# Kernel tuning notes

Measured on AMD Instinct MI355X. Metric: run time of the kernel, lower is better.

## Reference

```python
import jax, jax.numpy as jnp
import numpy as np

N, C, T, V = 32, 128, 128, 25
HS, HT, CI = 3, 2, 32
BN_INV = float(1.0 / np.sqrt(1.0 + 1e-5))  # eval-mode BN: running_mean=0, running_var=1


def conv1x1(x, w, b):
    # x: (N,C,T,V), w: (O,C), b: (O,)
    return jnp.einsum('nctv,oc->notv', x, w) + b[None, :, None, None]


def bn(x, g, b):
    return x * (g * BN_INV)[None, :, None, None] + b[None, :, None, None]


def lrelu(x):
    return jax.nn.leaky_relu(x, 0.1)


def setup_inputs() -> dict:
    key = jax.random.key(0)
    ks = jax.random.split(key, 16)
    w = lambda k, shp: jax.random.normal(k, shp, dtype=jnp.float32) * 0.05
    inp = {
        'x': jax.random.normal(ks[0], (N, C, T, V), dtype=jnp.float32),
        # spatial attention QK projection (conv 1x1): 2*HS*CI out channels
        'w_in_s': w(ks[1], (2 * HS * CI, C)), 'b_in_s': jnp.zeros((2 * HS * CI,), jnp.float32),
        'attention0s': jnp.ones((1, HS, V, V), jnp.float32) / V,
        'alphas': jnp.ones((1, HS, 1, 1), jnp.float32),
        'w_out_s': w(ks[2], (C, HS * C)), 'b_out_s': jnp.zeros((C,), jnp.float32),
        'g_out_s': jnp.ones((C,), jnp.float32), 'be_out_s': jnp.zeros((C,), jnp.float32),
        'w_ff_s': w(ks[3], (C, C)), 'b_ff_s': jnp.zeros((C,), jnp.float32),
        'g_ff_s': jnp.ones((C,), jnp.float32), 'be_ff_s': jnp.zeros((C,), jnp.float32),
        # temporal attention QK projection: 4*HT*CI out channels
        'w_in_t': w(ks[4], (4 * HT * CI, C)), 'b_in_t': jnp.zeros((4 * HT * CI,), jnp.float32),
        'alphat_f': jnp.ones((1, HT, 1, 1), jnp.float32),
        'alphat_b': jnp.ones((1, HT, 1, 1), jnp.float32),
        'w_out_t': w(ks[5], (C, 2 * HT * C)), 'b_out_t': jnp.zeros((C,), jnp.float32),
        'g_out_t': jnp.ones((C,), jnp.float32), 'be_out_t': jnp.zeros((C,), jnp.float32),
        'w_ff_t': w(ks[6], (C, C)), 'b_ff_t': jnp.zeros((C,), jnp.float32),
        'g_ff_t': jnp.ones((C,), jnp.float32), 'be_ff_t': jnp.zeros((C,), jnp.float32),
        # TCN: 7x1 temporal conv
        'w_tcn': w(ks[7], (C, C, 7, 1)), 'b_tcn': jnp.zeros((C,), jnp.float32),
        'g_tcn': jnp.ones((C,), jnp.float32), 'be_tcn': jnp.zeros((C,), jnp.float32),
    }
    return inp


def reference(x, w_in_s, b_in_s, attention0s, alphas, w_out_s, b_out_s, g_out_s, be_out_s,
              w_ff_s, b_ff_s, g_ff_s, be_ff_s, w_in_t, b_in_t, alphat_f, alphat_b,
              w_out_t, b_out_t, g_out_t, be_out_t, w_ff_t, b_ff_t, g_ff_t, be_ff_t,
              w_tcn, b_tcn, g_tcn, be_tcn):
    n = x.shape[0]
    # ---------------- spatial attention (S_atten='free', glo_reg_s) ----------------
    att_bias = attention0s[:, :, None]            # (1,HS,1,V,V) broadcast over T
    alphas_u = alphas[:, :, None]                 # (1,HS,1,1,1)
    qk = conv1x1(x, w_in_s, b_in_s).reshape(n, 2 * HS, CI, T, V)
    q, k = qk[:, :HS], qk[:, HS:]
    att = att_bias + jnp.tanh(jnp.einsum('nsctu,nsctv->nstuv', q, k) / CI) * alphas_u  # (N,HS,T,V,V)
    y = jnp.einsum('nctu,nstuv->nsctv', x, att).reshape(n, HS * C, T, V)
    y = bn(conv1x1(y, w_out_s, b_out_s), g_out_s, be_out_s)
    y = lrelu(x + y)                               # downs1 = identity (in==out, stride 1)
    y = bn(conv1x1(y, w_ff_s, b_ff_s), g_ff_s, be_ff_s)
    s_out = lrelu(x + y)                           # downs2 = identity
    # ---------------- temporal attention (directed, T_atten='context') ----------------
    z_in = s_out                                   # parallel=False -> temporal eats s_out
    qk_t = conv1x1(z_in, w_in_t, b_in_t).reshape(n, 4 * HT, CI, T, V)
    qt, kt = qk_t[:, :2 * HT], qk_t[:, 2 * HT:]
    qt = qt.mean(-1)                               # context attention: mean over joints -> (N,2HT,CI,T)
    kt = kt.mean(-1)
    att_t = jnp.tanh(jnp.einsum('nsct,nscu->nstu', qt, kt) / CI)  # (N,2HT,T,T)
    backward_mask = jnp.triu(jnp.ones((T, T), jnp.float32))
    forward_mask = backward_mask.T
    att_f = att_t[:, :HT] * alphat_f * forward_mask
    att_b = att_t[:, HT:] * alphat_b * backward_mask
    att_t = jnp.concatenate([att_f, att_b], axis=1)               # (N,2HT,T,T)
    z = jnp.einsum('nctv,nstu->nscuv', z_in, att_t).reshape(n, 2 * HT * C, T, V)
    z = bn(conv1x1(z, w_out_t, b_out_t), g_out_t, be_out_t)
    z = lrelu(z_in + z)                            # downt1 = identity
    z = bn(conv1x1(z, w_ff_t, b_ff_t), g_ff_t, be_ff_t)
    t_out = lrelu(z_in + z)                        # downt2 = identity
    # ---------------- TCN branch ----------------
    z2 = jax.lax.conv_general_dilated(t_out, w_tcn, (1, 1), ((3, 3), (0, 0)),
                                      dimension_numbers=('NCHW', 'OIHW', 'NCHW'))
    z2 = bn(z2 + b_tcn[None, :, None, None] * 0 + b_tcn[None, :, None, None], g_tcn, be_tcn) if False else bn(z2 + b_tcn[None, :, None, None], g_tcn, be_tcn)
    out = lrelu(t_out + z2)                        # downtTCN = identity
    return out
```

## Files before the change

### kernel.cpp

```cpp
#include <hip/hip_runtime.h>
#include <cstddef>

#define Nn 32
#define Cc 128
#define Tt 128
#define Vv 25
#define BN_INV 0.9999950000374997f


typedef __attribute__((ext_vector_type(8))) short bf16x8;
typedef __attribute__((ext_vector_type(4))) short short4v;
typedef __attribute__((ext_vector_type(4))) float f32x4;

__device__ __forceinline__ unsigned short f2bf(float f) {
    union { float f; unsigned u; } x; x.f = f;
    return (unsigned short)((x.u + 0x7FFFu + ((x.u >> 16) & 1u)) >> 16);
}
__device__ __forceinline__ float bf2f(unsigned short s) {
    union { unsigned u; float f; } x; x.u = ((unsigned)s) << 16;
    return x.f;
}


#define GFETCH(K0)                                                             \
    {                                                                          \
        int mg = m0 + sm;                                                      \
        if (mg < M) {                                                          \
            const unsigned short* ap = An + (size_t)mg*lda + (K0) + skh*16;    \
            a0n = *(const bf16x8*)ap;                                          \
            a1n = *(const bf16x8*)(ap + 8);                                    \
        }                                                                      \
        if (BMODE == 0) {                                                      \
            const unsigned short* Bn = (const unsigned short*)Bv               \
                                     + (size_t)n*bn_stride;                    \
            _Pragma("unroll")                                                  \
            for (int j = 0; j < 8; ++j)                                        \
                bqn[j] = Bn[(size_t)((K0) + skq*8 + j)*ldb + bcol];            \
        } else if (BMODE == 4) {                                               \
            const float* Bf = (const float*)Bv + (size_t)n*bn_stride;          \
            _Pragma("unroll")                                                  \
            for (int j = 0; j < 8; ++j)                                        \
                bqn[j] = f2bf(Bf[(size_t)((K0) + skq*8 + j)*ldb + bcol]);      \
        } else if (BMODE == 1) {                                               \
            const unsigned short* Bn = (const unsigned short*)Bv               \
                                     + (size_t)n*bn_stride;                    \
            int kb = (K0) + skq*8;                                             \
            int kidx = kb >> 7, c0 = kb & 127;                                 \
            int e = bcol + (kidx - 3)*25;                                      \
            bool ok = ((unsigned)e < 3200u);                                   \
            _Pragma("unroll")                                                  \
            for (int j = 0; j < 8; ++j)                                        \
                bqn[j] = ok ? Bn[(size_t)(c0 + j)*3200 + e] : (unsigned short)0;\
        } else if (BMODE == 3) {                                               \
            const unsigned short* Bn = (const unsigned short*)Bv               \
                                     + (size_t)n*bn_stride;                    \
            int kb = (K0) + skq*8;                                             \
            int h = kb >> 7, t0b = kb & 127;                                   \
            const unsigned short* bp = Bn + (size_t)h*409600 + (size_t)bo*3200 \
                                          + (size_t)t0b*25 + bv_;              \
            _Pragma("unroll")                                                  \
            for (int j = 0; j < 8; ++j) bqn[j] = bp[j*25];                     \
        } else if (BMODE == 6) {                                               \
            const unsigned short* Bn = (const unsigned short*)Bv               \
                                     + (size_t)n*bn_stride;                    \
            *(bf16x8*)bqn = *(const bf16x8*)(Bn + (size_t)bcol*ldb             \
                                             + (K0) + skq*8);                  \
        } else {                                                  \
            const unsigned short* Bn = (const unsigned short*)Bv               \
                                     + (size_t)n*bn_stride;                    \
            int kb = (K0) + skq*8;                                             \
            int kidx = kb >> 7, c0 = kb & 127;                                 \
            long e = (long)bcol + (long)(kidx - 3)*25;                         \
            *(bf16x8*)bqn = *(const bf16x8*)(Bn + e*128 + c0);                 \
        }                                                                      \
    }

template<int BMODE, int DMODE, int OM>
__global__ __launch_bounds__(256, 4) void gemm_k(
    const unsigned short* __restrict__ A, const void* __restrict__ Bv,
    float* __restrict__ D, unsigned short* __restrict__ Dbf,
    const float* __restrict__ resp, const float* __restrict__ bias,
    const float* __restrict__ gg, const float* __restrict__ bb,
    int M, int K, int lda, int ldb, int ldd,
    long an_stride, long bn_stride, long dn_stride, long dbfn,
    int gn, int gxn)
{
    __shared__ short Al[8*64*8];
    __shared__ short Bl[4*64*8];
    __shared__ __attribute__((aligned(16))) short Ot[(DMODE==1) ? 64*136 : 4];

    const int nwg = gridDim.x;
    const int b   = blockIdx.x;
    const int w   = (b & 7)*(nwg >> 3) + (b >> 3);
    const int n   = w / gxn;
    const int rem = w - n*gxn;
    const int mt  = rem / gn;
    const int nt  = rem - mt*gn;
    const int m0 = mt*128;
    const int j0 = nt*64;

    const unsigned short* An = A + (size_t)n*an_stride;

    const int tid = threadIdx.x;
    const int wav = tid >> 6, lane = tid & 63;
    const int lq = lane >> 4, l16 = lane & 15;

    const int sm  = tid >> 1, skh = tid & 1;
    const int scol = tid & 63, skq = tid >> 6;
    const int bcol = j0 + scol;

    int bo = 0, bv_ = 0;
    if (BMODE == 3) { bo = bcol/25; bv_ = bcol - 25*bo; }

    f32x4 acc[2][4];
    #pragma unroll
    for (int i = 0; i < 2; ++i)
        #pragma unroll
        for (int c = 0; c < 4; ++c) acc[i][c] = (f32x4){0.f,0.f,0.f,0.f};

    bf16x8 a0n = (bf16x8){0,0,0,0,0,0,0,0}, a1n = a0n;
    alignas(16) unsigned short bqn[8];
    GFETCH(0);

    for (int k0 = 0; k0 < K; k0 += 32) {
        __syncthreads();
        {
            short* Ap = Al + ((size_t)((sm>>4)*64 + (sm&15) + 32*skh))*8;
            *(bf16x8*)Ap = a0n;
            *(bf16x8*)(Ap + 128) = a1n;
        }
        {
            short* Bp = Bl + ((size_t)((scol>>4)*64 + skq*16 + (scol&15)))*8;
            *(bf16x8*)Bp = *(const bf16x8*)bqn;
        }
        __syncthreads();

        if (k0 + 32 < K) GFETCH(k0 + 32);

        bf16x8 afr[2], bfr[4];
        afr[0] = *(const bf16x8*)(Al + ((size_t)((2*wav+0)*64 + lane))*8);
        afr[1] = *(const bf16x8*)(Al + ((size_t)((2*wav+1)*64 + lane))*8);
        #pragma unroll
        for (int c = 0; c < 4; ++c)
            bfr[c] = *(const bf16x8*)(Bl + ((size_t)(c*64 + lane))*8);
        #pragma unroll
        for (int i = 0; i < 2; ++i)
            #pragma unroll
            for (int c = 0; c < 4; ++c)
                acc[i][c] = __builtin_amdgcn_mfma_f32_16x16x32_bf16(
                    afr[i], bfr[c], acc[i][c], 0, 0, 0);
    }

    if (DMODE == 1) {
        #pragma unroll
        for (int i = 0; i < 2; ++i) {
            const int mbase = (2*wav + i)*16 + lq*4;
            #pragma unroll
            for (int ct = 0; ct < 4; ++ct) {
                const int col = j0 + ct*16 + l16;
                short4v pk;
                #pragma unroll
                for (int r = 0; r < 4; ++r) {
                    const int mg = mbase + r;
                    const size_t addr = (size_t)mg*ldd + col + (size_t)n*dn_stride;
                    float val = acc[i][ct][r] + (bias ? bias[mg] : 0.f);
                    if (gg) {
                        val = val*(gg[mg]*BN_INV) + bb[mg] + resp[addr];
                        val = val > 0.f ? val : 0.1f*val;
                    }
                    if (OM != 1) D[addr] = val;
                    pk[r] = (short)f2bf(val);
                }
                *(short4v*)(Ot + (ct*16 + l16)*136 + mbase) = pk;
            }
        }
        __syncthreads();
        #pragma unroll
        for (int j = 0; j < 4; ++j) {
            int idx = j*256 + tid;
            int cl = idx >> 4, m8 = (idx & 15)*8;
            *(bf16x8*)(Dbf + (size_t)(j0 + cl)*128 + m8 + (size_t)n*dbfn)
                = *(const bf16x8*)(Ot + cl*136 + m8);
        }
    } else {
        #pragma unroll
        for (int i = 0; i < 2; ++i) {
            const int mbase = m0 + (2*wav + i)*16 + lq*4;
            #pragma unroll
            for (int ct = 0; ct < 4; ++ct) {
                const int col = j0 + ct*16 + l16;
                if (DMODE == 0) {
                    #pragma unroll
                    for (int r = 0; r < 4; ++r) {
                        const int mg = mbase + r;
                        if (mg < M) {
                            const size_t addr = (size_t)mg*ldd + col
                                              + (size_t)n*dn_stride;
                            float val = acc[i][ct][r] + (bias ? bias[mg] : 0.f);
                            if (gg) {
                                val = val*(gg[mg]*BN_INV) + bb[mg] + resp[addr];
                                val = val > 0.f ? val : 0.1f*val;
                            }
                            if (OM != 1) D[addr] = val;
                            if (OM >= 1) Dbf[addr] = f2bf(val);
                        }
                    }
                } else {
                    const int c = col/25, v = col - 25*c;
                    const float bi = bias ? bias[c] : 0.f;
                    float gv = 0.f, b2 = 0.f;
                    if (gg) { gv = gg[c]*BN_INV; b2 = bb[c]; }
                    #pragma unroll
                    for (int r = 0; r < 4; ++r) {
                        const int u = mbase + r;
                        const size_t addr = (size_t)c*3200 + (size_t)u*25 + v
                                          + (size_t)n*dn_stride;
                        float val = acc[i][ct][r] + bi;
                        if (gg) {
                            val = val*gv + b2 + resp[addr];
                            val = val > 0.f ? val : 0.1f*val;
                        }
                        if (OM != 1) D[addr] = val;
                        if (OM >= 1) Dbf[addr] = f2bf(val);
                    }
                }
            }
        }
    }
}

__global__ void k_prep(const float* __restrict__ wis, const float* __restrict__ wos,
                       const float* __restrict__ wfs, const float* __restrict__ wit,
                       const float* __restrict__ wot, const float* __restrict__ wft,
                       const float* __restrict__ wtc, unsigned short* __restrict__ W) {
    int i = blockIdx.x*256 + threadIdx.x;
    if (i < 24576) { W[i] = f2bf(wis[i]); return; }          i -= 24576;
    if (i < 49152) { W[24576 + i] = f2bf(wos[i]); return; }  i -= 49152;
    if (i < 16384) { W[73728 + i] = f2bf(wfs[i]); return; }  i -= 16384;
    if (i < 32768) { W[90112 + i] = f2bf(wit[i]); return; }  i -= 32768;
    if (i < 65536) {
        int ho = i >> 7, c = i & 127; int h = ho >> 7, o = ho & 127;
        W[122880 + i] = f2bf(wot[o*512 + h*128 + c]); return; } i -= 65536;
    if (i < 16384) { W[188416 + i] = f2bf(wft[i]); return; } i -= 16384;
    if (i < 114688) {
        int o = i / 896; int r = i - o*896; int kidx = r >> 7, c = r & 127;
        W[204800 + i] = f2bf(wtc[(o*128 + c)*7 + kidx]); }
}

__global__ void k_zpad(unsigned short* __restrict__ p) {
    int i = blockIdx.x*256 + threadIdx.x;
    if (i >= 76800) return;
    int chunk = i*8;
    int n = chunk / 19200;
    int r = chunk - n*19200;
    size_t addr = (size_t)n*428800 + (size_t)(r < 9600 ? r : 419200 + (r - 9600));
    *(bf16x8*)(p + addr) = (bf16x8){0,0,0,0,0,0,0,0};
}

__global__ void k_att_s(const unsigned short* __restrict__ qk,
                        const float* __restrict__ att0,
                        const float* __restrict__ alphas,
                        unsigned short* __restrict__ att) {
    int b = blockIdx.x;
    int n = b / (3*Tt); int rem = b - n*(3*Tt); int s = rem / Tt; int t = rem - s*Tt;
    __shared__ float qs[32*Vv], ks[32*Vv];
    const unsigned short* qp = qk + (size_t)n*614400 + (size_t)(s*32)*3200 + t*25;
    const unsigned short* kp = qk + (size_t)n*614400 + (size_t)(96 + s*32)*3200 + t*25;
    for (int i = threadIdx.x; i < 32*Vv; i += 256) {
        int c = i / Vv, v = i - c*Vv;
        qs[i] = bf2f(qp[(size_t)c*3200 + v]);
        ks[i] = bf2f(kp[(size_t)c*3200 + v]);
    }
    __syncthreads();
    float alpha = alphas[s];
    for (int i = threadIdx.x; i < Vv*Vv; i += 256) {
        int u = i / Vv, v = i - u*Vv;
        float a = 0.f;
        #pragma unroll
        for (int c = 0; c < 32; ++c) a += qs[c*Vv + u] * ks[c*Vv + v];
        att[(size_t)n*240000 + (size_t)s*80000 + (size_t)t*625 + i] =
            f2bf(att0[s*625 + i] + tanhf(a * (1.f/32.f)) * alpha);
    }
}

__global__ __launch_bounds__(256, 2) void k_eins_mfma(
    const float* __restrict__ X, const unsigned short* __restrict__ att,
    unsigned short* __restrict__ y2)
{
    __shared__ short Xf[128*128];
    __shared__ short Bf[7*4*64*8];

    const int n  = blockIdx.x >> 5;
    const int t0 = (blockIdx.x & 31) * 4;
    const int tid = threadIdx.x;
    const int wav = tid >> 6, lane = tid & 63;
    const int lq = lane >> 4, l16 = lane & 15;

    for (int i = tid; i < 7*4*64; i += 256)
        *(bf16x8*)(Bf + (size_t)i*8) = (bf16x8){0,0,0,0,0,0,0,0};

    const float* xp = X + (size_t)n*409600;
    for (int i = tid; i < 8192; i += 256) {
        int u2 = (i & 15)*2, tl = (i >> 4) & 3, c = i >> 6;
        float f0 = 0.f, f1 = 0.f;
        if (u2 < 25) {
            const float* p = xp + (size_t)c*3200 + (t0 + tl)*25 + u2;
            f0 = p[0];
            if (u2 < 24) f1 = p[1];
        }
        unsigned pk = (unsigned)f2bf(f0) | ((unsigned)f2bf(f1) << 16);
        int byte = (i*4) ^ ((c & 7) << 4);
        *(unsigned*)((char*)Xf + byte) = pk;
    }
    __syncthreads();

    bf16x8 afr[2][4];
    #pragma unroll
    for (int i = 0; i < 2; ++i) {
        const int c = (2*wav + i)*16 + l16;
        #pragma unroll
        for (int ks = 0; ks < 4; ++ks) {
            int byte = ((c*128 + ks*32 + lq*8)*2) ^ ((c & 7) << 4);
            afr[i][ks] = *(const bf16x8*)((const char*)Xf + byte);
        }
    }

    for (int s = 0; s < 3; ++s) {
        const unsigned short* ap = att + (size_t)n*240000 + (size_t)s*80000
                                       + (size_t)t0*625;
        for (int j = tid; j < 2500; j += 256) {
            int tl = j / 625, r = j - tl*625;
            int u = r / 25, v = r - u*25;
            int col = tl*25 + v;
            int l = ((u >> 3) << 4) | (col & 15);
            int nt = col >> 4;
            Bf[(size_t)((nt*4 + tl)*64 + l)*8 + (u & 7)] = (short)ap[j];
        }
        __syncthreads();

        f32x4 acc[2][7];
        #pragma unroll
        for (int i = 0; i < 2; ++i)
            #pragma unroll
            for (int nt = 0; nt < 7; ++nt) acc[i][nt] = (f32x4){0.f,0.f,0.f,0.f};

        #pragma unroll
        for (int ks = 0; ks < 4; ++ks) {
            bf16x8 bfr[7];
            #pragma unroll
            for (int nt = 0; nt < 7; ++nt)
                bfr[nt] = *(const bf16x8*)(Bf + (size_t)((nt*4 + ks)*64 + lane)*8);
            #pragma unroll
            for (int i = 0; i < 2; ++i)
                #pragma unroll
                for (int nt = 0; nt < 7; ++nt)
                    acc[i][nt] = __builtin_amdgcn_mfma_f32_16x16x32_bf16(
                        afr[i][ks], bfr[nt], acc[i][nt], 0, 0, 0);
        }

        unsigned short* yb = y2 + (size_t)n*1228800;
        #pragma unroll
        for (int i = 0; i < 2; ++i) {
            const int row = (2*wav + i)*16 + lq*4;
            #pragma unroll
            for (int nt = 0; nt < 7; ++nt) {
                const int col = nt*16 + l16;
                if (col < 100) {
                    short4v pk;
                    #pragma unroll
                    for (int r = 0; r < 4; ++r) pk[r] = (short)f2bf(acc[i][nt][r]);
                    *(short4v*)(yb + (size_t)(t0*25 + col)*384 + s*128 + row) = pk;
                }
            }
        }
        __syncthreads();
    }
}

__global__ void k_mean(const float* __restrict__ X, unsigned short* __restrict__ xb) {
    int idx = blockIdx.x*256 + threadIdx.x;
    if (idx >= Nn*Cc*Tt) return;
    const float* p = X + (size_t)idx*25;
    float s = 0.f;
    #pragma unroll
    for (int v = 0; v < Vv; ++v) s += p[v];
    int n = idx >> 14, rem = idx & 16383, c = rem >> 7, t = rem & 127;
    xb[(size_t)n*16384 + (size_t)t*128 + c] = f2bf(s * (1.f/25.f));
}

__global__ void k_att_t(const float* __restrict__ qkt, const float* __restrict__ af,
                        const float* __restrict__ ab, unsigned short* __restrict__ attb) {
    int n = blockIdx.x >> 2, h = blockIdx.x & 3;
    __shared__ float qs[32*Tt], ks[32*Tt];
    const float* qp = qkt + (size_t)n*32768 + (size_t)(h*32)*128;
    const float* kp = qkt + (size_t)n*32768 + (size_t)(128 + h*32)*128;
    for (int i = threadIdx.x; i < 32*Tt; i += 256) { qs[i] = qp[i]; ks[i] = kp[i]; }
    __syncthreads();
    float alpha = (h < 2) ? af[h] : ab[h-2];
    for (int i = threadIdx.x; i < Tt*Tt; i += 256) {
        int u = i >> 7, t = i & 127;
        bool keep = (h < 2) ? (t >= u) : (t <= u);
        float val = 0.f;
        if (keep) {
            float a = 0.f;
            #pragma unroll
            for (int c = 0; c < 32; ++c) a += qs[c*Tt + t] * ks[c*Tt + u];
            val = tanhf(a * (1.f/32.f)) * alpha;
        }
        attb[(size_t)n*65536 + (size_t)u*512 + h*128 + t] = f2bf(val);
    }
}

extern "C" void kernel_launch(void* const* d_in, const int* in_sizes, int n_in,
                              void* d_out, int out_size, void* d_ws, size_t ws_size,
                              hipStream_t stream) {
    const float* x       = (const float*)d_in[0];
    const float* w_in_s  = (const float*)d_in[1];
    const float* b_in_s  = (const float*)d_in[2];
    const float* att0s   = (const float*)d_in[3];
    const float* alphas  = (const float*)d_in[4];
    const float* w_out_s = (const float*)d_in[5];
    const float* b_out_s = (const float*)d_in[6];
    const float* g_out_s = (const float*)d_in[7];
    const float* be_out_s= (const float*)d_in[8];
    const float* w_ff_s  = (const float*)d_in[9];
    const float* b_ff_s  = (const float*)d_in[10];
    const float* g_ff_s  = (const float*)d_in[11];
    const float* be_ff_s = (const float*)d_in[12];
    const float* w_in_t  = (const float*)d_in[13];
    const float* b_in_t  = (const float*)d_in[14];
    const float* alphat_f= (const float*)d_in[15];
    const float* alphat_b= (const float*)d_in[16];
    const float* w_out_t = (const float*)d_in[17];
    const float* b_out_t = (const float*)d_in[18];
    const float* g_out_t = (const float*)d_in[19];
    const float* be_out_t= (const float*)d_in[20];
    const float* w_ff_t  = (const float*)d_in[21];
    const float* b_ff_t  = (const float*)d_in[22];
    const float* g_ff_t  = (const float*)d_in[23];
    const float* be_ff_t = (const float*)d_in[24];
    const float* w_tcn   = (const float*)d_in[25];
    const float* b_tcn   = (const float*)d_in[26];
    const float* g_tcn   = (const float*)d_in[27];
    const float* be_tcn  = (const float*)d_in[28];

    float* ws = (float*)d_ws;
    unsigned short* WB    = (unsigned short*)ws;
    unsigned short* QKBF  = (unsigned short*)(ws + 200000);
    unsigned short* S1BF  = (unsigned short*)(ws + 200000);
    unsigned short* ATSB  = (unsigned short*)(ws + 10030400);
    unsigned short* Y2BF  = (unsigned short*)(ws + 13870400);
    unsigned short* TOUTBP= (unsigned short*)(ws + 23710000);
    unsigned short* TOUTB = TOUTBP + 9600;
    float*          SOUT  = ws + 33531200;
    unsigned short* ATTB  = (unsigned short*)(ws + 200000);
    unsigned short* XBARB = (unsigned short*)(ws + 1300000);
    float*          QKT   = ws + 1600000;
    unsigned short* TMPB  = (unsigned short*)(ws + 2700000);
    unsigned short* T1BF  = (unsigned short*)(ws + 46638400);
    float*          TOUT  = ws + 2700000;
    float* out = (float*)d_out;

    unsigned short* wbis = WB;
    unsigned short* wbos = WB + 24576;
    unsigned short* wbfs = WB + 73728;
    unsigned short* wbit = WB + 90112;
    unsigned short* wbot = WB + 122880;
    unsigned short* wbft = WB + 188416;
    unsigned short* wbtc = WB + 204800;

    dim3 blk(256);
    const float* NUL = nullptr;

    k_prep<<<1248, blk, 0, stream>>>(w_in_s, w_out_s, w_ff_s, w_in_t,
                                     w_out_t, w_ff_t, w_tcn, WB);

    gemm_k<4,0,1><<<3200, blk, 0, stream>>>(
        wbis, x, nullptr, QKBF, NUL, b_in_s, NUL, NUL,
        192, 128, 128, 3200, 3200, 0L, 409600L, 614400L, 614400L, 50, 100);
    k_att_s<<<Nn*3*Tt, blk, 0, stream>>>(QKBF, att0s, alphas, ATSB);
    k_eins_mfma<<<dim3(Nn*32), blk, 0, stream>>>(x, ATSB, Y2BF);
    gemm_k<6,1,1><<<1600, blk, 0, stream>>>(
        wbos, Y2BF, nullptr, S1BF, x, b_out_s, g_out_s, be_out_s,
        128, 384, 384, 384, 3200, 0L, 1228800L, 409600L, 409600L, 50, 50);
    gemm_k<6,0,0><<<1600, blk, 0, stream>>>(
        wbfs, S1BF, SOUT, nullptr, x, b_ff_s, g_ff_s, be_ff_s,
        128, 128, 128, 128, 3200, 0L, 409600L, 409600L, 409600L, 50, 50);

    k_mean<<<2048, blk, 0, stream>>>(SOUT, XBARB);
    gemm_k<6,0,0><<<128, blk, 0, stream>>>(
        wbit, XBARB, QKT, nullptr, NUL, b_in_t, NUL, NUL,
        256, 128, 128, 128, 128, 0L, 16384L, 32768L, 32768L, 2, 4);
    k_att_t<<<Nn*4, blk, 0, stream>>>(QKT, alphat_f, alphat_b, ATTB);
    gemm_k<4,0,1><<<6400, blk, 0, stream>>>(
        wbot, SOUT, nullptr, TMPB, NUL, NUL, NUL, NUL,
        512, 128, 128, 3200, 3200, 0L, 409600L, 1638400L, 1638400L, 50, 200);
    gemm_k<3,2,1><<<1600, blk, 0, stream>>>(
        ATTB, TMPB, nullptr, T1BF, SOUT, b_out_t, g_out_t, be_out_t,
        128, 512, 512, 3200, 3200, 65536L, 1638400L, 409600L, 409600L, 50, 50);
    k_zpad<<<300, blk, 0, stream>>>(TOUTBP);
    gemm_k<0,1,2><<<1600, blk, 0, stream>>>(
        wbft, T1BF, TOUT, TOUTB, SOUT, b_ff_t, g_ff_t, be_ff_t,
        128, 128, 128, 3200, 3200, 0L, 409600L, 409600L, 428800L, 50, 50);

    gemm_k<7,0,0><<<1600, blk, 0, stream>>>(
        wbtc, TOUTB, out, nullptr, TOUT, b_tcn, g_tcn, be_tcn,
        128, 896, 896, 0, 3200, 0L, 428800L, 409600L, 409600L, 50, 50);
}
```

Baseline: 706.3 us.

## Add LDS-free register-direct MFMA GEMM for K-contiguous B operand modes

Adds a new GEMM kernel, gemm_nb, that loads A and B fragments straight from global memory into registers in MFMA operand layout. It skips LDS staging and block barriers in the main loop and double-buffers the loads across K steps. The K-contiguous launches (BMODE 6 and the TCN BMODE 7) now use it, and the now-unused B-mode branches are removed from the old kernel's fetch macro. This trades LDS traffic and syncs for redundant global/L2 loads across waves and less latency hiding.

```diff
diff --git a/kernel.cpp b/kernel.cpp
--- a/kernel.cpp
+++ b/kernel.cpp
@@ -21,6 +21,138 @@
     return x.f;
 }
 
+template<int BMODE, int DMODE, int OM>
+__global__ __launch_bounds__(256, 4) void gemm_nb(
+    const unsigned short* __restrict__ A, const void* __restrict__ Bv,
+    float* __restrict__ D, unsigned short* __restrict__ Dbf,
+    const float* __restrict__ resp, const float* __restrict__ bias,
+    const float* __restrict__ gg, const float* __restrict__ bb,
+    int M, int K, int lda, int ldb, int ldd,
+    long an_stride, long bn_stride, long dn_stride, long dbfn,
+    int gn, int gxn)
+{
+    __shared__ __attribute__((aligned(16))) short Ot[(DMODE==1) ? 64*136 : 4];
+
+    const int nwg = gridDim.x;
+    const int b   = blockIdx.x;
+    const int w   = (b & 7)*(nwg >> 3) + (b >> 3);
+    const int n   = w / gxn;
+    const int rem = w - n*gxn;
+    const int mt  = rem / gn;
+    const int nt  = rem - mt*gn;
+    const int m0 = mt*128;
+    const int j0 = nt*64;
+
+    const int tid = threadIdx.x;
+    const int wav = tid >> 6, lane = tid & 63;
+    const int lq = lane >> 4, l16 = lane & 15;
+
+    const unsigned short* An = A + (size_t)n*an_stride;
+    const unsigned short* Bn = (const unsigned short*)Bv + (size_t)n*bn_stride;
+
+    const unsigned short* pa0 = An + (size_t)(m0 + (2*wav+0)*16 + l16)*lda + lq*8;
+    const unsigned short* pa1 = An + (size_t)(m0 + (2*wav+1)*16 + l16)*lda + lq*8;
+    const unsigned short* pb[4];
+    #pragma unroll
+    for (int c = 0; c < 4; ++c) {
+        const int col = j0 + c*16 + l16;
+        pb[c] = (BMODE == 6) ? Bn + (size_t)col*ldb + lq*8
+                             : Bn + ((long)col - 75)*128 + lq*8;
+    }
+
+    f32x4 acc[2][4];
+    #pragma unroll
+    for (int i = 0; i < 2; ++i)
+        #pragma unroll
+        for (int c = 0; c < 4; ++c) acc[i][c] = (f32x4){0.f,0.f,0.f,0.f};
+
+#define OFFB(K0) ((BMODE == 6) ? (long)(K0) \
+                               : ((long)((K0) >> 7)*3200 + (long)((K0) & 127)))
+#define LOADF(K0, A0, A1, BF)                                                  \
+    {                                                                          \
+        A0 = *(const bf16x8*)(pa0 + (K0));                                     \
+        A1 = *(const bf16x8*)(pa1 + (K0));                                     \
+        const long ob = OFFB(K0);                                              \
+        _Pragma("unroll")                                                      \
+        for (int c = 0; c < 4; ++c) BF[c] = *(const bf16x8*)(pb[c] + ob);      \
+    }
+#define MFMA8(A0, A1, BF)                                                      \
+    {                                                                          \
+        _Pragma("unroll")                                                      \
+        for (int c = 0; c < 4; ++c) {                                          \
+            acc[0][c] = __builtin_amdgcn_mfma_f32_16x16x32_bf16(               \
+                A0, BF[c], acc[0][c], 0, 0, 0);                                \
+            acc[1][c] = __builtin_amdgcn_mfma_f32_16x16x32_bf16(               \
+                A1, BF[c], acc[1][c], 0, 0, 0);                                \
+        }                                                                      \
+    }
+
+    bf16x8 aA0, aA1, bA[4], aB0, aB1, bB[4];
+    LOADF(0, aA0, aA1, bA);
+    for (int k0 = 0; k0 < K; k0 += 64) {
+        if (k0 + 32 < K) LOADF(k0 + 32, aB0, aB1, bB);
+        MFMA8(aA0, aA1, bA);
+        if (k0 + 64 < K) LOADF(k0 + 64, aA0, aA1, bA);
+        if (k0 + 32 < K) MFMA8(aB0, aB1, bB);
+    }
+#undef OFFB
+#undef LOADF
+#undef MFMA8
+
+    if (DMODE == 1) {
+        #pragma unroll
+        for (int i = 0; i < 2; ++i) {
+            const int mbase = (2*wav + i)*16 + lq*4;
+            #pragma unroll
+            for (int ct = 0; ct < 4; ++ct) {
+                const int col = j0 + ct*16 + l16;
+                short4v pk;
+                #pragma unroll
+                for (int r = 0; r < 4; ++r) {
+                    const int mg = mbase + r;
+                    const size_t addr = (size_t)mg*ldd + col + (size_t)n*dn_stride;
+                    float val = acc[i][ct][r] + (bias ? bias[mg] : 0.f);
+                    if (gg) {
+                        val = val*(gg[mg]*BN_INV) + bb[mg] + resp[addr];
+                        val = val > 0.f ? val : 0.1f*val;
+                    }
+                    if (OM != 1) D[addr] = val;
+                    pk[r] = (short)f2bf(val);
+                }
+                *(short4v*)(Ot + (ct*16 + l16)*136 + mbase) = pk;
+            }
+        }
+        __syncthreads();
+        #pragma unroll
+        for (int j = 0; j < 4; ++j) {
+            int idx = j*256 + tid;
+            int cl = idx >> 4, m8 = (idx & 15)*8;
+            *(bf16x8*)(Dbf + (size_t)(j0 + cl)*128 + m8 + (size_t)n*dbfn)
+                = *(const bf16x8*)(Ot + cl*136 + m8);
+        }
+    } else {
+        #pragma unroll
+        for (int i = 0; i < 2; ++i) {
+            const int mbase = m0 + (2*wav + i)*16 + lq*4;
+            #pragma unroll
+            for (int ct = 0; ct < 4; ++ct) {
+                const int col = j0 + ct*16 + l16;
+                #pragma unroll
+                for (int r = 0; r < 4; ++r) {
+                    const int mg = mbase + r;
+                    const size_t addr = (size_t)mg*ldd + col + (size_t)n*dn_stride;
+                    float val = acc[i][ct][r] + (bias ? bias[mg] : 0.f);
+                    if (gg) {
+                        val = val*(gg[mg]*BN_INV) + bb[mg] + resp[addr];
+                        val = val > 0.f ? val : 0.1f*val;
+                    }
+                    if (OM != 1) D[addr] = val;
+                    if (OM >= 1) Dbf[addr] = f2bf(val);
+                }
+            }
+        }
+    }
+}
 
 #define GFETCH(K0)                                                             \
     {                                                                          \
@@ -41,17 +173,7 @@
             _Pragma("unroll")                                                  \
             for (int j = 0; j < 8; ++j)                                        \
                 bqn[j] = f2bf(Bf[(size_t)((K0) + skq*8 + j)*ldb + bcol]);      \
-        } else if (BMODE == 1) {                                               \
-            const unsigned short* Bn = (const unsigned short*)Bv               \
-                                     + (size_t)n*bn_stride;                    \
-            int kb = (K0) + skq*8;                                             \
-            int kidx = kb >> 7, c0 = kb & 127;                                 \
-            int e = bcol + (kidx - 3)*25;                                      \
-            bool ok = ((unsigned)e < 3200u);                                   \
-            _Pragma("unroll")                                                  \
-            for (int j = 0; j < 8; ++j)                                        \
-                bqn[j] = ok ? Bn[(size_t)(c0 + j)*3200 + e] : (unsigned short)0;\
-        } else if (BMODE == 3) {                                               \
+        } else {                                                  \
             const unsigned short* Bn = (const unsigned short*)Bv               \
                                      + (size_t)n*bn_stride;                    \
             int kb = (K0) + skq*8;                                             \
@@ -60,18 +182,6 @@
                                           + (size_t)t0b*25 + bv_;              \
             _Pragma("unroll")                                                  \
             for (int j = 0; j < 8; ++j) bqn[j] = bp[j*25];                     \
-        } else if (BMODE == 6) {                                               \
-            const unsigned short* Bn = (const unsigned short*)Bv               \
-                                     + (size_t)n*bn_stride;                    \
-            *(bf16x8*)bqn = *(const bf16x8*)(Bn + (size_t)bcol*ldb             \
-                                             + (K0) + skq*8);                  \
-        } else {                                                  \
-            const unsigned short* Bn = (const unsigned short*)Bv               \
-                                     + (size_t)n*bn_stride;                    \
-            int kb = (K0) + skq*8;                                             \
-            int kidx = kb >> 7, c0 = kb & 127;                                 \
-            long e = (long)bcol + (long)(kidx - 3)*25;                         \
-            *(bf16x8*)bqn = *(const bf16x8*)(Bn + e*128 + c0);                 \
         }                                                                      \
     }
 
@@ -480,15 +590,15 @@
         192, 128, 128, 3200, 3200, 0L, 409600L, 614400L, 614400L, 50, 100);
     k_att_s<<<Nn*3*Tt, blk, 0, stream>>>(QKBF, att0s, alphas, ATSB);
     k_eins_mfma<<<dim3(Nn*32), blk, 0, stream>>>(x, ATSB, Y2BF);
-    gemm_k<6,1,1><<<1600, blk, 0, stream>>>(
+    gemm_nb<6,1,1><<<1600, blk, 0, stream>>>(
         wbos, Y2BF, nullptr, S1BF, x, b_out_s, g_out_s, be_out_s,
         128, 384, 384, 384, 3200, 0L, 1228800L, 409600L, 409600L, 50, 50);
-    gemm_k<6,0,0><<<1600, blk, 0, stream>>>(
+    gemm_nb<6,0,0><<<1600, blk, 0, stream>>>(
         wbfs, S1BF, SOUT, nullptr, x, b_ff_s, g_ff_s, be_ff_s,
         128, 128, 128, 128, 3200, 0L, 409600L, 409600L, 409600L, 50, 50);
 
     k_mean<<<2048, blk, 0, stream>>>(SOUT, XBARB);
-    gemm_k<6,0,0><<<128, blk, 0, stream>>>(
+    gemm_nb<6,0,0><<<128, blk, 0, stream>>>(
         wbit, XBARB, QKT, nullptr, NUL, b_in_t, NUL, NUL,
         256, 128, 128, 128, 128, 0L, 16384L, 32768L, 32768L, 2, 4);
     k_att_t<<<Nn*4, blk, 0, stream>>>(QKT, alphat_f, alphat_b, ATTB);
@@ -503,7 +613,7 @@
         wbft, T1BF, TOUT, TOUTB, SOUT, b_ff_t, g_ff_t, be_ff_t,
         128, 128, 128, 3200, 3200, 0L, 409600L, 409600L, 428800L, 50, 50);
 
-    gemm_k<7,0,0><<<1600, blk, 0, stream>>>(
+    gemm_nb<7,0,0><<<1600, blk, 0, stream>>>(
         wbtc, TOUTB, out, nullptr, TOUT, b_tcn, g_tcn, be_tcn,
         128, 896, 896, 0, 3200, 0L, 428800L, 409600L, 409600L, 50, 50);
 }
```

New measurement: 800.7 us. 13.4% more time.

## Fuse spatial out-projection and feedforward GEMMs into one kernel via LDS

Applied to the files above, without the earlier changes.

Replaces the two back-to-back spatial-branch GEMMs (out projection with BN/residual/leaky-relu, then feedforward 1x1 conv) with a single kernel. The intermediate bf16 tile stays in LDS and feeds the second MFMA GEMM directly instead of going through global memory. This removes one launch and the write and read of the S1 intermediate. In exchange the kernel uses more LDS and registers per block, and the unused BMODE 1 path is deleted.

```diff
diff --git a/kernel.cpp b/kernel.cpp
--- a/kernel.cpp
+++ b/kernel.cpp
@@ -20,7 +20,6 @@
     union { unsigned u; float f; } x; x.u = ((unsigned)s) << 16;
     return x.f;
 }
-
 
 #define GFETCH(K0)                                                             \
     {                                                                          \
@@ -41,16 +40,6 @@
             _Pragma("unroll")                                                  \
             for (int j = 0; j < 8; ++j)                                        \
                 bqn[j] = f2bf(Bf[(size_t)((K0) + skq*8 + j)*ldb + bcol]);      \
-        } else if (BMODE == 1) {                                               \
-            const unsigned short* Bn = (const unsigned short*)Bv               \
-                                     + (size_t)n*bn_stride;                    \
-            int kb = (K0) + skq*8;                                             \
-            int kidx = kb >> 7, c0 = kb & 127;                                 \
-            int e = bcol + (kidx - 3)*25;                                      \
-            bool ok = ((unsigned)e < 3200u);                                   \
-            _Pragma("unroll")                                                  \
-            for (int j = 0; j < 8; ++j)                                        \
-                bqn[j] = ok ? Bn[(size_t)(c0 + j)*3200 + e] : (unsigned short)0;\
         } else if (BMODE == 3) {                                               \
             const unsigned short* Bn = (const unsigned short*)Bv               \
                                      + (size_t)n*bn_stride;                    \
@@ -229,6 +218,150 @@
     }
 }
 
+__global__ __launch_bounds__(256, 4) void k_s1ff(
+    const unsigned short* __restrict__ A1, const unsigned short* __restrict__ B1,
+    const unsigned short* __restrict__ A2,
+    float* __restrict__ D, const float* __restrict__ xresp,
+    const float* __restrict__ b1, const float* __restrict__ g1,
+    const float* __restrict__ bb1,
+    const float* __restrict__ b2, const float* __restrict__ g2,
+    const float* __restrict__ bb2)
+{
+    __shared__ short Al[8*64*8];
+    __shared__ short Bl[4*64*8];
+    __shared__ __attribute__((aligned(16))) short Ilds[64*136];
+
+    const int nwg = gridDim.x;
+    const int b   = blockIdx.x;
+    const int w   = (b & 7)*(nwg >> 3) + (b >> 3);
+    const int n   = w / 50;
+    const int nt  = w - n*50;
+    const int j0  = nt*64;
+
+    const int tid = threadIdx.x;
+    const int wav = tid >> 6, lane = tid & 63;
+    const int lq = lane >> 4, l16 = lane & 15;
+
+    const int sm  = tid >> 1, skh = tid & 1;
+    const int scol = tid & 63, skq = tid >> 6;
+    const int bcol = j0 + scol;
+
+    const unsigned short* Bn = B1 + (size_t)n*1228800;
+
+    f32x4 acc[2][4];
+    #pragma unroll
+    for (int i = 0; i < 2; ++i)
+        #pragma unroll
+        for (int c = 0; c < 4; ++c) acc[i][c] = (f32x4){0.f,0.f,0.f,0.f};
+
+    bf16x8 a0n, a1n;
+    alignas(16) unsigned short bqn[8];
+    {
+        const unsigned short* ap = A1 + (size_t)sm*384 + skh*16;
+        a0n = *(const bf16x8*)ap;
+        a1n = *(const bf16x8*)(ap + 8);
+        *(bf16x8*)bqn = *(const bf16x8*)(Bn + (size_t)bcol*384 + skq*8);
+    }
+
+    for (int k0 = 0; k0 < 384; k0 += 32) {
+        __syncthreads();
+        {
+            short* Ap = Al + ((size_t)((sm>>4)*64 + (sm&15) + 32*skh))*8;
+            *(bf16x8*)Ap = a0n;
+            *(bf16x8*)(Ap + 128) = a1n;
+        }
+        {
+            short* Bp = Bl + ((size_t)((scol>>4)*64 + skq*16 + (scol&15)))*8;
+            *(bf16x8*)Bp = *(const bf16x8*)bqn;
+        }
+        __syncthreads();
+
+        if (k0 + 32 < 384) {
+            const unsigned short* ap = A1 + (size_t)sm*384 + (k0+32) + skh*16;
+            a0n = *(const bf16x8*)ap;
+            a1n = *(const bf16x8*)(ap + 8);
+            *(bf16x8*)bqn = *(const bf16x8*)(Bn + (size_t)bcol*384 + (k0+32) + skq*8);
+        }
+
+        bf16x8 afr[2], bfr[4];
+        afr[0] = *(const bf16x8*)(Al + ((size_t)((2*wav+0)*64 + lane))*8);
+        afr[1] = *(const bf16x8*)(Al + ((size_t)((2*wav+1)*64 + lane))*8);
+        #pragma unroll
+        for (int c = 0; c < 4; ++c)
+            bfr[c] = *(const bf16x8*)(Bl + ((size_t)(c*64 + lane))*8);
+        #pragma unroll
+        for (int i = 0; i < 2; ++i)
+            #pragma unroll
+            for (int c = 0; c < 4; ++c)
+                acc[i][c] = __builtin_amdgcn_mfma_f32_16x16x32_bf16(
+                    afr[i], bfr[c], acc[i][c], 0, 0, 0);
+    }
+
+    __syncthreads();
+    #pragma unroll
+    for (int i = 0; i < 2; ++i) {
+        const int mbase = (2*wav + i)*16 + lq*4;
+        #pragma unroll
+        for (int ct = 0; ct < 4; ++ct) {
+            const int col = j0 + ct*16 + l16;
+            short4v pk;
+            #pragma unroll
+            for (int r = 0; r < 4; ++r) {
+                const int mg = mbase + r;
+                const size_t addr = (size_t)mg*3200 + col + (size_t)n*409600;
+                float val = acc[i][ct][r] + b1[mg];
+                val = val*(g1[mg]*BN_INV) + bb1[mg] + xresp[addr];
+                val = val > 0.f ? val : 0.1f*val;
+                pk[r] = (short)f2bf(val);
+            }
+            *(short4v*)(Ilds + (ct*16 + l16)*136 + mbase) = pk;
+        }
+    }
+    __syncthreads();
+
+    f32x4 acc2[2][4];
+    #pragma unroll
+    for (int i = 0; i < 2; ++i)
+        #pragma unroll
+        for (int c = 0; c < 4; ++c) acc2[i][c] = (f32x4){0.f,0.f,0.f,0.f};
+
+    #pragma unroll
+    for (int k2 = 0; k2 < 128; k2 += 32) {
+        bf16x8 a2[2], b2f[4];
+        #pragma unroll
+        for (int i = 0; i < 2; ++i)
+            a2[i] = *(const bf16x8*)(A2 + (size_t)((2*wav+i)*16 + l16)*128
+                                        + k2 + lq*8);
+        #pragma unroll
+        for (int c = 0; c < 4; ++c)
+            b2f[c] = *(const bf16x8*)(Ilds + (c*16 + l16)*136 + k2 + lq*8);
+        #pragma unroll
+        for (int i = 0; i < 2; ++i)
+            #pragma unroll
+            for (int c = 0; c < 4; ++c)
+                acc2[i][c] = __builtin_amdgcn_mfma_f32_16x16x32_bf16(
+                    a2[i], b2f[c], acc2[i][c], 0, 0, 0);
+    }
+
+    #pragma unroll
+    for (int i = 0; i < 2; ++i) {
+        const int mbase = (2*wav + i)*16 + lq*4;
+        #pragma unroll
+        for (int ct = 0; ct < 4; ++ct) {
+            const int col = j0 + ct*16 + l16;
+            #pragma unroll
+            for (int r = 0; r < 4; ++r) {
+                const int mg = mbase + r;
+                const size_t addr = (size_t)mg*3200 + col + (size_t)n*409600;
+                float val = acc2[i][ct][r] + b2[mg];
+                val = val*(g2[mg]*BN_INV) + bb2[mg] + xresp[addr];
+                val = val > 0.f ? val : 0.1f*val;
+                D[addr] = val;
+            }
+        }
+    }
+}
+
 __global__ void k_prep(const float* __restrict__ wis, const float* __restrict__ wos,
                        const float* __restrict__ wfs, const float* __restrict__ wit,
                        const float* __restrict__ wot, const float* __restrict__ wft,
@@ -447,7 +580,6 @@
     float* ws = (float*)d_ws;
     unsigned short* WB    = (unsigned short*)ws;
     unsigned short* QKBF  = (unsigned short*)(ws + 200000);
-    unsigned short* S1BF  = (unsigned short*)(ws + 200000);
     unsigned short* ATSB  = (unsigned short*)(ws + 10030400);
     unsigned short* Y2BF  = (unsigned short*)(ws + 13870400);
     unsigned short* TOUTBP= (unsigned short*)(ws + 23710000);
@@ -480,12 +612,9 @@
         192, 128, 128, 3200, 3200, 0L, 409600L, 614400L, 614400L, 50, 100);
     k_att_s<<<Nn*3*Tt, blk, 0, stream>>>(QKBF, att0s, alphas, ATSB);
     k_eins_mfma<<<dim3(Nn*32), blk, 0, stream>>>(x, ATSB, Y2BF);
-    gemm_k<6,1,1><<<1600, blk, 0, stream>>>(
-        wbos, Y2BF, nullptr, S1BF, x, b_out_s, g_out_s, be_out_s,
-        128, 384, 384, 384, 3200, 0L, 1228800L, 409600L, 409600L, 50, 50);
-    gemm_k<6,0,0><<<1600, blk, 0, stream>>>(
-        wbfs, S1BF, SOUT, nullptr, x, b_ff_s, g_ff_s, be_ff_s,
-        128, 128, 128, 128, 3200, 0L, 409600L, 409600L, 409600L, 50, 50);
+    k_s1ff<<<1600, blk, 0, stream>>>(
+        wbos, Y2BF, wbfs, SOUT, x,
+        b_out_s, g_out_s, be_out_s, b_ff_s, g_ff_s, be_ff_s);
 
     k_mean<<<2048, blk, 0, stream>>>(SOUT, XBARB);
     gemm_k<6,0,0><<<128, blk, 0, stream>>>(
```

After: 647.9 us. 8.3% less time.
